# Performance work log

Measured on AMD Instinct MI355X. Metric: run time of the kernel, lower is better.

The kernel has to match this reference:

```python
import jax, jax.numpy as jnp
import numpy as np

B, Q, K, D = 32, 1024, 1024, 128

def setup_inputs() -> dict:
    key = jax.random.key(0)
    kq, kk, kv, kl = jax.random.split(key, 4)
    return {
        "queries": jax.random.normal(kq, (B, Q, D), dtype=jnp.float32),
        "keys": jax.random.normal(kk, (B, K, D), dtype=jnp.float32),
        "values": jax.random.normal(kv, (B, K, D), dtype=jnp.float32),
        "valid_length": jax.random.randint(kl, (B,), 1, K + 1),
    }

def reference(queries, keys, values, valid_length):
    d = queries.shape[-1]
    # scores: [B, Q, K]
    scores = jnp.einsum("bqd,bkd->bqk", queries, keys) / jnp.sqrt(jnp.float32(d))
    # length mask: position k is valid iff k < valid_length[b]
    mask = jnp.arange(keys.shape[1])[None, None, :] < valid_length[:, None, None]
    scores = jnp.where(mask, scores, jnp.float32(-1e9))
    attn = jax.nn.softmax(scores, axis=-1)
    # dropout module is identity in eval / p=0
    return jnp.einsum("bqk,bkv->bqv", attn, values)
```

## Files before the change

### kernel.cpp

```cpp
#include <hip/hip_runtime.h>
#include <hip/hip_bf16.h>
#include <stdint.h>

#define B_    32
#define QLEN  1024
#define KSEQ  1024
#define DIM   128
#define NKT   (KSEQ / 64)
#define SCALE 0.08838834764831845f

typedef __attribute__((ext_vector_type(8)))  short short8;
typedef __attribute__((ext_vector_type(4)))  float floatx4;
typedef __attribute__((ext_vector_type(16))) float floatx16;
typedef unsigned int u32;

__device__ __forceinline__ u32 f2bf(float x) {
  union { float f; u32 u; } v; v.f = x;
  return (v.u + 0x7FFF + ((v.u >> 16) & 1)) >> 16;
}
__device__ __forceinline__ u32 pack2(float lo, float hi) {
  return f2bf(lo) | (f2bf(hi) << 16);
}
__device__ __forceinline__ u32 cvtpk(float lo, float hi) {
  u32 d;
  asm("v_cvt_pk_bf16_f32 %0, %1, %2" : "=v"(d) : "v"(lo), "v"(hi));
  return d;
}
__device__ __forceinline__ void swap32(u32& a, u32& b) {
  asm volatile("v_permlane32_swap_b32 %0, %1" : "+v"(a), "+v"(b));
}
typedef union { uint4 u; short8 s; } U8;

__device__ __forceinline__ void barrier_full() {
  asm volatile("s_waitcnt vmcnt(0) lgkmcnt(0)" ::: "memory");
  __syncthreads();
}

__global__ __launch_bounds__(256) void prep_kernel(const float* __restrict__ Kg,
                                                   const float* __restrict__ Vg,
                                                   const int* __restrict__ vlen,
                                                   uint4* __restrict__ Ksw,
                                                   uint4* __restrict__ Vsw,
                                                   int2* __restrict__ task) {
  __shared__ __align__(16) u32 Vu[64 * 65];
  __shared__ int sidx[32];
  const int kt = blockIdx.x, b = blockIdx.y, t = threadIdx.x;
  const bool tableblk = (blockIdx.z == 0) && (kt == 0) && (b == 0);

  if (tableblk && t < 64) {
    const int bb = t & 31;
    const int ntb = (vlen[bb] + 63) >> 6;
    int rank = 0;
#pragma unroll
    for (int j = 0; j < 32; j++) {
      const int ntj = __shfl(ntb, j);
      rank += (ntj > ntb) | ((ntj == ntb) & (j < bb));
    }
    if (t < 32) sidx[rank] = bb;
  }

  if (kt * 64 < vlen[b]) {
    if (blockIdx.z == 0) {
      const float* src = Kg + ((size_t)b * KSEQ + kt * 64) * DIM;
      uint4* dst = Ksw + ((size_t)b * NKT + kt) * 1024;
#pragma unroll
      for (int it = 0; it < 4; it++) {
        const int f = it * 256 + t, r = f >> 4, c = f & 15;
        floatx4 f0 = *(const floatx4*)(src + r * DIM + c * 8);
        floatx4 f1 = *(const floatx4*)(src + r * DIM + c * 8 + 4);
        uint4 o;
        o.x = pack2(f0[0], f0[1]); o.y = pack2(f0[2], f0[3]);
        o.z = pack2(f1[0], f1[1]); o.w = pack2(f1[2], f1[3]);
        dst[r * 16 + (c ^ (r & 15))] = o;
      }
    } else {
      const float* src = Vg + ((size_t)b * KSEQ + kt * 64) * DIM;
#pragma unroll
      for (int it = 0; it < 8; it++) {
        const int k = it * 8 + (t >> 5), c = t & 31;
        const floatx4 f = *(const floatx4*)(src + (size_t)k * DIM + c * 4);
        const int s = (k >> 3) & 4;
        Vu[k * 65 + ((2 * c) ^ s)]     = pack2(f[0], f[1]);
        Vu[k * 65 + ((2 * c + 1) ^ s)] = pack2(f[2], f[3]);
      }
      __syncthreads();
      uint4* dst = Vsw + ((size_t)b * NKT + kt) * 1024;
#pragma unroll
      for (int it = 0; it < 4; it++) {
        const int id = it * 256 + t;
        const int kc = id & 7, d = (id >> 3) & 127;
        const int col = (d >> 1) ^ (kc & 4);
        u32 r[8];
#pragma unroll
        for (int j = 0; j < 8; j++) r[j] = Vu[(kc * 8 + j) * 65 + col];
        const u32 sel = (d & 1) ? 0x07060302u : 0x05040100u;
        uint4 o;
        o.x = __builtin_amdgcn_perm(r[1], r[0], sel);
        o.y = __builtin_amdgcn_perm(r[3], r[2], sel);
        o.z = __builtin_amdgcn_perm(r[5], r[4], sel);
        o.w = __builtin_amdgcn_perm(r[7], r[6], sel);
        dst[d * 8 + (kc ^ (d & 7))] = o;
      }
    }
  }

  if (tableblk) {
    __syncthreads();
    for (int l = t; l < 512; l += 256) {
      const int x = l & 7, j = l >> 3;
      int rank, q;
      if (j < 32) { rank = (j & 1) ? x + 8  : x;      q = j >> 1; }
      else        { rank = (j & 1) ? x + 16 : x + 24; q = (j - 32) >> 1; }
      task[l] = make_int2(sidx[rank], q << 6);
    }
  }
}

typedef const __attribute__((address_space(1))) u32* as1p;
typedef __attribute__((address_space(3))) u32* as3p;
__device__ __forceinline__ void gl_lds16(const void* g, void* l) {
  __builtin_amdgcn_global_load_lds((as1p)g, (as3p)l, 16, 0, 0);
}

__global__ __launch_bounds__(256, 2) void attn_kernel(
    const float* __restrict__ Qg, const uint4* __restrict__ Ksw,
    const uint4* __restrict__ Vsw, const int* __restrict__ vlen,
    const int2* __restrict__ task, float* __restrict__ Og) {
  __shared__ __align__(16) short Kbuf[2][64 * 128];
  __shared__ float Lred[2][32];

  const int2 tq = task[blockIdx.x];
  const int b = tq.x, q0 = tq.y;
  const int t = threadIdx.x, wave = t >> 6, lane = t & 63;
  const int qh = wave & 1, kh = wave >> 1;
  const int l31 = lane & 31, hi = lane >> 5, m15 = l31 & 15, m7 = l31 & 7;
  const int L  = vlen[b];
  const int nt = (L + 63) >> 6;

  const char*  Kt = (const char*)(Ksw + (size_t)b * NKT * 1024);
  const short* Vt = (const short*)(Vsw + (size_t)b * NKT * 1024);

  short8 qb[8];
  {
    const float* qrow = Qg + ((size_t)b * QLEN + q0 + qh * 32 + l31) * DIM;
#pragma unroll
    for (int c = 0; c < 8; c++) {
      floatx4 f0 = *(const floatx4*)(qrow + c * 16 + hi * 8);
      floatx4 f1 = *(const floatx4*)(qrow + c * 16 + hi * 8 + 4);
      short8 a;
      a[0] = (short)f2bf(f0[0]); a[1] = (short)f2bf(f0[1]);
      a[2] = (short)f2bf(f0[2]); a[3] = (short)f2bf(f0[3]);
      a[4] = (short)f2bf(f1[0]); a[5] = (short)f2bf(f1[1]);
      a[6] = (short)f2bf(f1[2]); a[7] = (short)f2bf(f1[3]);
      qb[c] = a;
    }
  }

  float lrow = 0.0f;
  floatx16 oacc[4];
#pragma unroll
  for (int dt = 0; dt < 4; dt++)
#pragma unroll
    for (int i = 0; i < 16; i++) oacc[dt][i] = 0.0f;

#define ISSUE_K(tk, bb)                                                        \
  {                                                                            \
    const char* g_ = Kt + (size_t)(tk) * 16384 + wave * 4096 + lane * 16;      \
    _Pragma("unroll") for (int i_ = 0; i_ < 4; i_++)                           \
        gl_lds16(g_ + i_ * 1024, (char*)Kbuf[bb] + wave * 4096 + i_ * 1024);   \
  }

  ISSUE_K(0, 0);

  for (int tk = 0; tk < nt; tk++) {
    const int k0 = tk * 64;
    barrier_full();
    if (tk + 1 < nt) ISSUE_K(tk + 1, (tk + 1) & 1);
    const short* Kb_ = Kbuf[tk & 1];

    short8 vb[4][2];
    {
      const short* vt_ = Vt + (size_t)tk * 8192;
#pragma unroll
      for (int dt = 0; dt < 4; dt++) {
        const short* vr_ = vt_ + (dt * 32 + l31) * 64;
        vb[dt][0] = *(const short8*)(vr_ + ((kh * 4 + 0 + hi) ^ m7) * 8);
        vb[dt][1] = *(const short8*)(vr_ + ((kh * 4 + 2 + hi) ^ m7) * 8);
      }
    }

    floatx16 s;
#pragma unroll
    for (int i = 0; i < 16; i++) s[i] = 0.0f;
    {
      const short* kr = Kb_ + (kh * 32 + l31) * 128;
      __builtin_amdgcn_s_setprio(1);
#pragma unroll
      for (int c = 0; c < 8; c++) {
        const short8 ka = *(const short8*)(kr + ((2 * c + hi) ^ m15) * 8);
        s = __builtin_amdgcn_mfma_f32_32x32x16_bf16(ka, qb[c], s, 0, 0, 0);
      }
      __builtin_amdgcn_s_setprio(0);
    }

    if (k0 + kh * 32 + 32 <= L) {
#pragma unroll
      for (int r = 0; r < 16; r++) {
        s[r] = __expf(fminf(s[r] * SCALE, 30.0f));
        lrow += s[r];
      }
    } else {
#pragma unroll
      for (int r = 0; r < 16; r++) {
        const int ck = (r & 3) + 8 * (r >> 2) + 4 * hi;
        const float a = (k0 + kh * 32 + ck < L)
                            ? __expf(fminf(s[r] * SCALE, 30.0f)) : 0.0f;
        s[r] = a;
        lrow += a;
      }
    }

    {
      u32 u0 = cvtpk(s[0], s[1]),   u1 = cvtpk(s[2], s[3]);
      u32 u2 = cvtpk(s[4], s[5]),   u3 = cvtpk(s[6], s[7]);
      swap32(u0, u2); swap32(u1, u3);
      u32 w0 = cvtpk(s[8], s[9]),   w1 = cvtpk(s[10], s[11]);
      u32 w2 = cvtpk(s[12], s[13]), w3 = cvtpk(s[14], s[15]);
      swap32(w0, w2); swap32(w1, w3);
      U8 pu0; pu0.u.x = u0; pu0.u.y = u1; pu0.u.z = u2; pu0.u.w = u3;
      U8 pu1; pu1.u.x = w0; pu1.u.y = w1; pu1.u.z = w2; pu1.u.w = w3;
      __builtin_amdgcn_s_setprio(1);
#pragma unroll
      for (int dt = 0; dt < 4; dt++) {
        oacc[dt] = __builtin_amdgcn_mfma_f32_32x32x16_bf16(pu0.s, vb[dt][0], oacc[dt], 0, 0, 0);
        oacc[dt] = __builtin_amdgcn_mfma_f32_32x32x16_bf16(pu1.s, vb[dt][1], oacc[dt], 0, 0, 0);
      }
      __builtin_amdgcn_s_setprio(0);
    }
  }

  lrow += __shfl_xor(lrow, 32);
  barrier_full();
  float* scr = (float*)Kbuf;
  if (kh == 1) {
    if (lane < 32) Lred[qh][l31] = lrow;
#pragma unroll
    for (int dt = 0; dt < 4; dt++)
#pragma unroll
      for (int r = 0; r < 16; r++)
        scr[(dt * 16 + r) * 128 + qh * 64 + lane] = oacc[dt][r];
  }
  __syncthreads();
  if (kh == 0) {
    const float ltot = lrow + Lred[qh][l31];
    const float inv_ = 1.0f / ltot;
    float iv[16];
#pragma unroll
    for (int r = 0; r < 16; r++)
      iv[r] = __shfl(inv_, (r & 3) + 8 * (r >> 2) + 4 * hi);
    float* obase = Og + ((size_t)b * QLEN + q0 + qh * 32) * DIM + l31;
#pragma unroll
    for (int dt = 0; dt < 4; dt++) {
#pragma unroll
      for (int r = 0; r < 16; r++) {
        const int rq = (r & 3) + 8 * (r >> 2) + 4 * hi;
        const float v = oacc[dt][r] + scr[(dt * 16 + r) * 128 + qh * 64 + lane];
        obase[(size_t)rq * DIM + dt * 32] = v * iv[r];
      }
    }
  }
#undef ISSUE_K
}

extern "C" void kernel_launch(void* const* d_in, const int* in_sizes, int n_in,
                              void* d_out, int out_size, void* d_ws, size_t ws_size,
                              hipStream_t stream) {
  const float* Qg = (const float*)d_in[0];
  const float* Kg = (const float*)d_in[1];
  const float* Vg = (const float*)d_in[2];
  const int*  vln = (const int*)d_in[3];
  uint4* Ksw = (uint4*)d_ws;
  uint4* Vsw = (uint4*)((char*)d_ws + (size_t)B_ * NKT * 16384);
  int2*  Tsk = (int2*)((char*)d_ws + 2 * (size_t)B_ * NKT * 16384);

  prep_kernel<<<dim3(NKT, B_, 2), 256, 0, stream>>>(Kg, Vg, vln, Ksw, Vsw, Tsk);
  attn_kernel<<<dim3(512), 256, 0, stream>>>(Qg, Ksw, Vsw, vln, Tsk,
                                             (float*)d_out);
}
```

Before: 116.8 us.

## Load K tiles directly to registers with double-buffered prefetch, drop LDS staging

Replaces the LDS-staged, barrier-synchronised K tile pipeline (global_load_lds into two shared buffers) with per-lane direct global loads into register double buffers, prefetching the next tile while computing the current one. This removes the per-iteration block barrier and the LDS round trip for K. In exchange it raises register pressure (16 extra short8 registers), which could hurt occupancy at launch bounds of 2 blocks per CU, and each wave now fetches its own K rows from global/L2, so K rows are read redundantly by the two qh waves.

```diff
diff --git a/kernel.cpp b/kernel.cpp
--- a/kernel.cpp
+++ b/kernel.cpp
@@ -30,11 +30,6 @@
   asm volatile("v_permlane32_swap_b32 %0, %1" : "+v"(a), "+v"(b));
 }
 typedef union { uint4 u; short8 s; } U8;
-
-__device__ __forceinline__ void barrier_full() {
-  asm volatile("s_waitcnt vmcnt(0) lgkmcnt(0)" ::: "memory");
-  __syncthreads();
-}
 
 __global__ __launch_bounds__(256) void prep_kernel(const float* __restrict__ Kg,
                                                    const float* __restrict__ Vg,
@@ -116,17 +111,11 @@
   }
 }
 
-typedef const __attribute__((address_space(1))) u32* as1p;
-typedef __attribute__((address_space(3))) u32* as3p;
-__device__ __forceinline__ void gl_lds16(const void* g, void* l) {
-  __builtin_amdgcn_global_load_lds((as1p)g, (as3p)l, 16, 0, 0);
-}
-
 __global__ __launch_bounds__(256, 2) void attn_kernel(
     const float* __restrict__ Qg, const uint4* __restrict__ Ksw,
     const uint4* __restrict__ Vsw, const int* __restrict__ vlen,
     const int2* __restrict__ task, float* __restrict__ Og) {
-  __shared__ __align__(16) short Kbuf[2][64 * 128];
+  __shared__ float scr[64 * 128];
   __shared__ float Lred[2][32];
 
   const int2 tq = task[blockIdx.x];
@@ -136,9 +125,10 @@
   const int l31 = lane & 31, hi = lane >> 5, m15 = l31 & 15, m7 = l31 & 7;
   const int L  = vlen[b];
   const int nt = (L + 63) >> 6;
-
-  const char*  Kt = (const char*)(Ksw + (size_t)b * NKT * 1024);
-  const short* Vt = (const short*)(Vsw + (size_t)b * NKT * 1024);
+  const int krow = kh * 32 + l31;
+
+  const short* KtS = (const short*)(Ksw + (size_t)b * NKT * 1024);
+  const short* Vt  = (const short*)(Vsw + (size_t)b * NKT * 1024);
 
   short8 qb[8];
   {
@@ -163,85 +153,78 @@
 #pragma unroll
     for (int i = 0; i < 16; i++) oacc[dt][i] = 0.0f;
 
-#define ISSUE_K(tk, bb)                                                        \
+#define LOAD_K(DST, tkv)                                                       \
   {                                                                            \
-    const char* g_ = Kt + (size_t)(tk) * 16384 + wave * 4096 + lane * 16;      \
-    _Pragma("unroll") for (int i_ = 0; i_ < 4; i_++)                           \
-        gl_lds16(g_ + i_ * 1024, (char*)Kbuf[bb] + wave * 4096 + i_ * 1024);   \
-  }
-
-  ISSUE_K(0, 0);
-
-  for (int tk = 0; tk < nt; tk++) {
-    const int k0 = tk * 64;
-    barrier_full();
-    if (tk + 1 < nt) ISSUE_K(tk + 1, (tk + 1) & 1);
-    const short* Kb_ = Kbuf[tk & 1];
-
-    short8 vb[4][2];
-    {
-      const short* vt_ = Vt + (size_t)tk * 8192;
-#pragma unroll
-      for (int dt = 0; dt < 4; dt++) {
-        const short* vr_ = vt_ + (dt * 32 + l31) * 64;
-        vb[dt][0] = *(const short8*)(vr_ + ((kh * 4 + 0 + hi) ^ m7) * 8);
-        vb[dt][1] = *(const short8*)(vr_ + ((kh * 4 + 2 + hi) ^ m7) * 8);
-      }
-    }
-
-    floatx16 s;
-#pragma unroll
-    for (int i = 0; i < 16; i++) s[i] = 0.0f;
-    {
-      const short* kr = Kb_ + (kh * 32 + l31) * 128;
-      __builtin_amdgcn_s_setprio(1);
-#pragma unroll
-      for (int c = 0; c < 8; c++) {
-        const short8 ka = *(const short8*)(kr + ((2 * c + hi) ^ m15) * 8);
-        s = __builtin_amdgcn_mfma_f32_32x32x16_bf16(ka, qb[c], s, 0, 0, 0);
-      }
-      __builtin_amdgcn_s_setprio(0);
-    }
-
-    if (k0 + kh * 32 + 32 <= L) {
-#pragma unroll
-      for (int r = 0; r < 16; r++) {
-        s[r] = __expf(fminf(s[r] * SCALE, 30.0f));
-        lrow += s[r];
-      }
-    } else {
-#pragma unroll
-      for (int r = 0; r < 16; r++) {
-        const int ck = (r & 3) + 8 * (r >> 2) + 4 * hi;
-        const float a = (k0 + kh * 32 + ck < L)
-                            ? __expf(fminf(s[r] * SCALE, 30.0f)) : 0.0f;
-        s[r] = a;
-        lrow += a;
-      }
-    }
-
-    {
-      u32 u0 = cvtpk(s[0], s[1]),   u1 = cvtpk(s[2], s[3]);
-      u32 u2 = cvtpk(s[4], s[5]),   u3 = cvtpk(s[6], s[7]);
-      swap32(u0, u2); swap32(u1, u3);
-      u32 w0 = cvtpk(s[8], s[9]),   w1 = cvtpk(s[10], s[11]);
-      u32 w2 = cvtpk(s[12], s[13]), w3 = cvtpk(s[14], s[15]);
-      swap32(w0, w2); swap32(w1, w3);
-      U8 pu0; pu0.u.x = u0; pu0.u.y = u1; pu0.u.z = u2; pu0.u.w = u3;
-      U8 pu1; pu1.u.x = w0; pu1.u.y = w1; pu1.u.z = w2; pu1.u.w = w3;
-      __builtin_amdgcn_s_setprio(1);
-#pragma unroll
-      for (int dt = 0; dt < 4; dt++) {
-        oacc[dt] = __builtin_amdgcn_mfma_f32_32x32x16_bf16(pu0.s, vb[dt][0], oacc[dt], 0, 0, 0);
-        oacc[dt] = __builtin_amdgcn_mfma_f32_32x32x16_bf16(pu1.s, vb[dt][1], oacc[dt], 0, 0, 0);
-      }
-      __builtin_amdgcn_s_setprio(0);
-    }
+    const short* kp_ = KtS + (size_t)(tkv) * 8192 + krow * 128;                \
+    _Pragma("unroll") for (int c_ = 0; c_ < 8; c_++)                           \
+      DST[c_] = *(const short8*)(kp_ + ((2 * c_ + hi) ^ m15) * 8);             \
+  }
+
+#define BODY(KF, tkv)                                                          \
+  {                                                                            \
+    const int k0_ = (tkv) * 64;                                                \
+    short8 vb[4][2];                                                           \
+    {                                                                          \
+      const short* vt_ = Vt + (size_t)(tkv) * 8192;                            \
+      _Pragma("unroll") for (int dt = 0; dt < 4; dt++) {                       \
+        const short* vr_ = vt_ + (dt * 32 + l31) * 64;                         \
+        vb[dt][0] = *(const short8*)(vr_ + ((kh * 4 + 0 + hi) ^ m7) * 8);      \
+        vb[dt][1] = *(const short8*)(vr_ + ((kh * 4 + 2 + hi) ^ m7) * 8);      \
+      }                                                                        \
+    }                                                                          \
+    floatx16 s;                                                                \
+    _Pragma("unroll") for (int i = 0; i < 16; i++) s[i] = 0.0f;                \
+    __builtin_amdgcn_s_setprio(1);                                             \
+    _Pragma("unroll") for (int c = 0; c < 8; c++)                              \
+      s = __builtin_amdgcn_mfma_f32_32x32x16_bf16(KF[c], qb[c], s, 0, 0, 0);   \
+    __builtin_amdgcn_s_setprio(0);                                             \
+    if (k0_ + kh * 32 + 32 <= L) {                                             \
+      _Pragma("unroll") for (int r = 0; r < 16; r++) {                         \
+        s[r] = __expf(fminf(s[r] * SCALE, 30.0f));                             \
+        lrow += s[r];                                                          \
+      }                                                                        \
+    } else {                                                                   \
+      _Pragma("unroll") for (int r = 0; r < 16; r++) {                         \
+        const int ck = (r & 3) + 8 * (r >> 2) + 4 * hi;                        \
+        const float a = (k0_ + kh * 32 + ck < L)                               \
+                            ? __expf(fminf(s[r] * SCALE, 30.0f)) : 0.0f;       \
+        s[r] = a;                                                              \
+        lrow += a;                                                             \
+      }                                                                        \
+    }                                                                          \
+    {                                                                          \
+      u32 u0 = cvtpk(s[0], s[1]),   u1 = cvtpk(s[2], s[3]);                    \
+      u32 u2 = cvtpk(s[4], s[5]),   u3 = cvtpk(s[6], s[7]);                    \
+      swap32(u0, u2); swap32(u1, u3);                                          \
+      u32 w0 = cvtpk(s[8], s[9]),   w1 = cvtpk(s[10], s[11]);                  \
+      u32 w2 = cvtpk(s[12], s[13]), w3 = cvtpk(s[14], s[15]);                  \
+      swap32(w0, w2); swap32(w1, w3);                                          \
+      U8 pu0; pu0.u.x = u0; pu0.u.y = u1; pu0.u.z = u2; pu0.u.w = u3;          \
+      U8 pu1; pu1.u.x = w0; pu1.u.y = w1; pu1.u.z = w2; pu1.u.w = w3;          \
+      __builtin_amdgcn_s_setprio(1);                                           \
+      _Pragma("unroll") for (int dt = 0; dt < 4; dt++) {                       \
+        oacc[dt] = __builtin_amdgcn_mfma_f32_32x32x16_bf16(pu0.s, vb[dt][0],   \
+                                                           oacc[dt], 0, 0, 0);\
+        oacc[dt] = __builtin_amdgcn_mfma_f32_32x32x16_bf16(pu1.s, vb[dt][1],   \
+                                                           oacc[dt], 0, 0, 0);\
+      }                                                                        \
+      __builtin_amdgcn_s_setprio(0);                                           \
+    }                                                                          \
+  }
+
+  short8 ka[8], kb[8];
+  LOAD_K(ka, 0);
+  int tk = 0;
+  for (;;) {
+    if (tk + 1 < nt) LOAD_K(kb, tk + 1);
+    BODY(ka, tk);
+    if (++tk == nt) break;
+    if (tk + 1 < nt) LOAD_K(ka, tk + 1);
+    BODY(kb, tk);
+    if (++tk == nt) break;
   }
 
   lrow += __shfl_xor(lrow, 32);
-  barrier_full();
-  float* scr = (float*)Kbuf;
   if (kh == 1) {
     if (lane < 32) Lred[qh][l31] = lrow;
 #pragma unroll
@@ -269,7 +252,8 @@
       }
     }
   }
-#undef ISSUE_K
+#undef LOAD_K
+#undef BODY
 }
 
 extern "C" void kernel_launch(void* const* d_in, const int* in_sizes, int n_in,
```

New measurement: 116.7 us. Within noise of the previous version (-0.1%).

## Prelayout K/V in fragment order, stage V via LDS, fold scale into K

Applied to the files above, without the earlier changes.

The prep kernel now multiplies K by the softmax scale times log2(e) and writes both K and V in the exact per-lane MFMA fragment order. The attention kernel can then read them with linear, conflict-free LDS loads, and V is double-buffered into LDS through async global_load_lds instead of being read straight from global memory. The exponential becomes a raw v_exp_f32 (exp2) with no clamp and no per-element scale multiply, and the row-sum is done as a tree reduction. LDS use rises to 64KB per block, which may limit occupancy at two blocks per CU. Dropping the clamp at 30 risks overflow for large scores, since there is no max subtraction.

```diff
diff --git a/kernel.cpp b/kernel.cpp
--- a/kernel.cpp
+++ b/kernel.cpp
@@ -7,7 +7,7 @@
 #define KSEQ  1024
 #define DIM   128
 #define NKT   (KSEQ / 64)
-#define SCALE 0.08838834764831845f
+#define KSC   0.12751879522655792f
 
 typedef __attribute__((ext_vector_type(8)))  short short8;
 typedef __attribute__((ext_vector_type(4)))  float floatx4;
@@ -28,6 +28,11 @@
 }
 __device__ __forceinline__ void swap32(u32& a, u32& b) {
   asm volatile("v_permlane32_swap_b32 %0, %1" : "+v"(a), "+v"(b));
+}
+__device__ __forceinline__ float exp2_fast(float x) {
+  float d;
+  asm("v_exp_f32 %0, %1" : "=v"(d) : "v"(x));
+  return d;
 }
 typedef union { uint4 u; short8 s; } U8;
 
@@ -43,6 +48,7 @@
                                                    uint4* __restrict__ Vsw,
                                                    int2* __restrict__ task) {
   __shared__ __align__(16) u32 Vu[64 * 65];
+  __shared__ __align__(16) uint4 Ku[64 * 17];
   __shared__ int sidx[32];
   const int kt = blockIdx.x, b = blockIdx.y, t = threadIdx.x;
   const bool tableblk = (blockIdx.z == 0) && (kt == 0) && (b == 0);
@@ -62,16 +68,25 @@
   if (kt * 64 < vlen[b]) {
     if (blockIdx.z == 0) {
       const float* src = Kg + ((size_t)b * KSEQ + kt * 64) * DIM;
-      uint4* dst = Ksw + ((size_t)b * NKT + kt) * 1024;
 #pragma unroll
       for (int it = 0; it < 4; it++) {
         const int f = it * 256 + t, r = f >> 4, c = f & 15;
         floatx4 f0 = *(const floatx4*)(src + r * DIM + c * 8);
         floatx4 f1 = *(const floatx4*)(src + r * DIM + c * 8 + 4);
         uint4 o;
-        o.x = pack2(f0[0], f0[1]); o.y = pack2(f0[2], f0[3]);
-        o.z = pack2(f1[0], f1[1]); o.w = pack2(f1[2], f1[3]);
-        dst[r * 16 + (c ^ (r & 15))] = o;
+        o.x = pack2(f0[0] * KSC, f0[1] * KSC); o.y = pack2(f0[2] * KSC, f0[3] * KSC);
+        o.z = pack2(f1[0] * KSC, f1[1] * KSC); o.w = pack2(f1[2] * KSC, f1[3] * KSC);
+        Ku[r * 17 + c] = o;
+      }
+      __syncthreads();
+      uint4* dst = Ksw + ((size_t)b * NKT + kt) * 1024;
+#pragma unroll
+      for (int it = 0; it < 4; it++) {
+        const int o16 = it * 256 + t;
+        const int kh = o16 >> 9, cs = (o16 >> 6) & 7, lane = o16 & 63;
+        const int hi = lane >> 5, l31 = lane & 31;
+        const int r = kh * 32 + l31, j = 2 * cs + hi;
+        dst[o16] = Ku[r * 17 + j];
       }
     } else {
       const float* src = Vg + ((size_t)b * KSEQ + kt * 64) * DIM;
@@ -87,8 +102,12 @@
       uint4* dst = Vsw + ((size_t)b * NKT + kt) * 1024;
 #pragma unroll
       for (int it = 0; it < 4; it++) {
-        const int id = it * 256 + t;
-        const int kc = id & 7, d = (id >> 3) & 127;
+        const int o16 = it * 256 + t;
+        const int kh = o16 >> 9, slot = (o16 >> 6) & 7, lane = o16 & 63;
+        const int dt = slot >> 1, i_ = slot & 1;
+        const int hi = lane >> 5, l31 = lane & 31;
+        const int d = dt * 32 + l31;
+        const int kc = (kh * 4 + 2 * i_ + hi);
         const int col = (d >> 1) ^ (kc & 4);
         u32 r[8];
 #pragma unroll
@@ -99,7 +118,7 @@
         o.y = __builtin_amdgcn_perm(r[3], r[2], sel);
         o.z = __builtin_amdgcn_perm(r[5], r[4], sel);
         o.w = __builtin_amdgcn_perm(r[7], r[6], sel);
-        dst[d * 8 + (kc ^ (d & 7))] = o;
+        dst[o16] = o;
       }
     }
   }
@@ -126,19 +145,19 @@
     const float* __restrict__ Qg, const uint4* __restrict__ Ksw,
     const uint4* __restrict__ Vsw, const int* __restrict__ vlen,
     const int2* __restrict__ task, float* __restrict__ Og) {
-  __shared__ __align__(16) short Kbuf[2][64 * 128];
+  __shared__ __align__(16) char SMEM[65536];
   __shared__ float Lred[2][32];
 
   const int2 tq = task[blockIdx.x];
   const int b = tq.x, q0 = tq.y;
   const int t = threadIdx.x, wave = t >> 6, lane = t & 63;
   const int qh = wave & 1, kh = wave >> 1;
-  const int l31 = lane & 31, hi = lane >> 5, m15 = l31 & 15, m7 = l31 & 7;
+  const int l31 = lane & 31, hi = lane >> 5;
   const int L  = vlen[b];
   const int nt = (L + 63) >> 6;
 
-  const char*  Kt = (const char*)(Ksw + (size_t)b * NKT * 1024);
-  const short* Vt = (const short*)(Vsw + (size_t)b * NKT * 1024);
+  const char* KtI = (const char*)(Ksw + (size_t)b * NKT * 1024);
+  const char* VtI = (const char*)(Vsw + (size_t)b * NKT * 1024);
 
   short8 qb[8];
   {
@@ -165,60 +184,63 @@
 
 #define ISSUE_K(tk, bb)                                                        \
   {                                                                            \
-    const char* g_ = Kt + (size_t)(tk) * 16384 + wave * 4096 + lane * 16;      \
+    const char* g_ = KtI + (size_t)(tk) * 16384 + wave * 4096 + lane * 16;     \
     _Pragma("unroll") for (int i_ = 0; i_ < 4; i_++)                           \
-        gl_lds16(g_ + i_ * 1024, (char*)Kbuf[bb] + wave * 4096 + i_ * 1024);   \
+        gl_lds16(g_ + i_ * 1024, SMEM + (bb) * 16384 + wave * 4096 + i_ * 1024); \
+  }
+#define ISSUE_V(tk, bb)                                                        \
+  {                                                                            \
+    const char* g_ = VtI + (size_t)(tk) * 16384 + wave * 4096 + lane * 16;     \
+    _Pragma("unroll") for (int i_ = 0; i_ < 4; i_++)                           \
+        gl_lds16(g_ + i_ * 1024,                                               \
+                 SMEM + 32768 + (bb) * 16384 + wave * 4096 + i_ * 1024);       \
   }
 
   ISSUE_K(0, 0);
+  ISSUE_V(0, 0);
 
   for (int tk = 0; tk < nt; tk++) {
     const int k0 = tk * 64;
+    const int bb = tk & 1;
     barrier_full();
-    if (tk + 1 < nt) ISSUE_K(tk + 1, (tk + 1) & 1);
-    const short* Kb_ = Kbuf[tk & 1];
-
+    if (tk + 1 < nt) {
+      ISSUE_K(tk + 1, bb ^ 1);
+      ISSUE_V(tk + 1, bb ^ 1);
+    }
+
+    const short* Kl_ = (const short*)(SMEM + bb * 16384) + kh * 4096 + lane * 8;
+    const short* Vl_ = (const short*)(SMEM + 32768 + bb * 16384) + kh * 4096 + lane * 8;
+    short8 kf[8];
+#pragma unroll
+    for (int c = 0; c < 8; c++) kf[c] = *(const short8*)(Kl_ + c * 512);
     short8 vb[4][2];
-    {
-      const short* vt_ = Vt + (size_t)tk * 8192;
-#pragma unroll
-      for (int dt = 0; dt < 4; dt++) {
-        const short* vr_ = vt_ + (dt * 32 + l31) * 64;
-        vb[dt][0] = *(const short8*)(vr_ + ((kh * 4 + 0 + hi) ^ m7) * 8);
-        vb[dt][1] = *(const short8*)(vr_ + ((kh * 4 + 2 + hi) ^ m7) * 8);
-      }
+#pragma unroll
+    for (int dt = 0; dt < 4; dt++) {
+      vb[dt][0] = *(const short8*)(Vl_ + (dt * 2 + 0) * 512);
+      vb[dt][1] = *(const short8*)(Vl_ + (dt * 2 + 1) * 512);
     }
 
     floatx16 s;
 #pragma unroll
     for (int i = 0; i < 16; i++) s[i] = 0.0f;
-    {
-      const short* kr = Kb_ + (kh * 32 + l31) * 128;
-      __builtin_amdgcn_s_setprio(1);
-#pragma unroll
-      for (int c = 0; c < 8; c++) {
-        const short8 ka = *(const short8*)(kr + ((2 * c + hi) ^ m15) * 8);
-        s = __builtin_amdgcn_mfma_f32_32x32x16_bf16(ka, qb[c], s, 0, 0, 0);
-      }
-      __builtin_amdgcn_s_setprio(0);
-    }
+    __builtin_amdgcn_s_setprio(1);
+#pragma unroll
+    for (int c = 0; c < 8; c++)
+      s = __builtin_amdgcn_mfma_f32_32x32x16_bf16(kf[c], qb[c], s, 0, 0, 0);
+    __builtin_amdgcn_s_setprio(0);
 
     if (k0 + kh * 32 + 32 <= L) {
 #pragma unroll
-      for (int r = 0; r < 16; r++) {
-        s[r] = __expf(fminf(s[r] * SCALE, 30.0f));
-        lrow += s[r];
-      }
+      for (int r = 0; r < 16; r++) s[r] = exp2_fast(s[r]);
     } else {
 #pragma unroll
       for (int r = 0; r < 16; r++) {
         const int ck = (r & 3) + 8 * (r >> 2) + 4 * hi;
-        const float a = (k0 + kh * 32 + ck < L)
-                            ? __expf(fminf(s[r] * SCALE, 30.0f)) : 0.0f;
-        s[r] = a;
-        lrow += a;
-      }
-    }
+        s[r] = (k0 + kh * 32 + ck < L) ? exp2_fast(s[r]) : 0.0f;
+      }
+    }
+    lrow += (((s[0] + s[1]) + (s[2] + s[3])) + ((s[4] + s[5]) + (s[6] + s[7]))) +
+            (((s[8] + s[9]) + (s[10] + s[11])) + ((s[12] + s[13]) + (s[14] + s[15])));
 
     {
       u32 u0 = cvtpk(s[0], s[1]),   u1 = cvtpk(s[2], s[3]);
@@ -232,8 +254,10 @@
       __builtin_amdgcn_s_setprio(1);
 #pragma unroll
       for (int dt = 0; dt < 4; dt++) {
-        oacc[dt] = __builtin_amdgcn_mfma_f32_32x32x16_bf16(pu0.s, vb[dt][0], oacc[dt], 0, 0, 0);
-        oacc[dt] = __builtin_amdgcn_mfma_f32_32x32x16_bf16(pu1.s, vb[dt][1], oacc[dt], 0, 0, 0);
+        oacc[dt] = __builtin_amdgcn_mfma_f32_32x32x16_bf16(pu0.s, vb[dt][0],
+                                                           oacc[dt], 0, 0, 0);
+        oacc[dt] = __builtin_amdgcn_mfma_f32_32x32x16_bf16(pu1.s, vb[dt][1],
+                                                           oacc[dt], 0, 0, 0);
       }
       __builtin_amdgcn_s_setprio(0);
     }
@@ -241,7 +265,7 @@
 
   lrow += __shfl_xor(lrow, 32);
   barrier_full();
-  float* scr = (float*)Kbuf;
+  float* scr = (float*)SMEM;
   if (kh == 1) {
     if (lane < 32) Lred[qh][l31] = lrow;
 #pragma unroll
@@ -270,6 +294,7 @@
     }
   }
 #undef ISSUE_K
+#undef ISSUE_V
 }
 
 extern "C" void kernel_launch(void* const* d_in, const int* in_sizes, int n_in,
```

Measured after the change: 114.6 us. No clear change (-1.9%).
